# Kernel tuning notes

Measured on AMD Instinct MI355X. Metric: run time of the kernel, lower is better.

The kernel has to match this reference:

```python
import jax, jax.numpy as jnp
import numpy as np

B = 16384        # batch size
K = 50           # neighbors per user (fixed for static shapes)
T = B * K        # total gathered neighbor items
NNEG = 20        # negative samples per positive
D = 128          # embedding dim
N_USERS = 100000
N_ITEMS = 100000
ALPHA = 1.0


def setup_inputs() -> dict:
    key = jax.random.key(0)
    k = jax.random.split(key, 9)
    I = jax.random.randint(k[0], (B,), 0, N_ITEMS)
    U = jax.random.randint(k[1], (B,), 0, N_USERS)
    I_neg = jax.random.randint(k[2], (B, NNEG), 0, N_ITEMS)
    I_U = jax.random.randint(k[3], (T,), 0, N_ITEMS)
    N_U = jnp.full((B,), K, dtype=jnp.int32)
    I_in_I_U = jax.random.randint(k[4], (B,), 0, 2).astype(jnp.int32)
    P_emb = jax.random.normal(k[5], (N_ITEMS, D), jnp.float32) * 0.02
    Q_emb = jax.random.normal(k[6], (N_ITEMS, D), jnp.float32) * 0.02
    b_u = jax.random.normal(k[7], (N_USERS,), jnp.float32) * 0.01
    b_i = jax.random.normal(k[8], (N_ITEMS,), jnp.float32) * 0.01
    return {"I": I, "U": U, "I_neg": I_neg, "I_U": I_U, "N_U": N_U,
            "I_in_I_U": I_in_I_U, "P_emb": P_emb, "Q_emb": Q_emb,
            "b_u": b_u, "b_i": b_i}


def reference(I, U, I_neg, I_U, N_U, I_in_I_U, P_emb, Q_emb, b_u, b_i):
    # P(.) / Q(.) abstracted as embedding lookups
    q = Q_emb[I]                     # [B, D]
    p = P_emb[I_U]                   # [T, D]
    p_self = P_emb[I]                # [B, D]

    # scatter-add neighbor embeddings into per-row sums
    U_idx = jnp.repeat(jnp.arange(B), N_U, total_repeat_length=T)  # [T]
    p_sum = jax.ops.segment_sum(p, U_idx, num_segments=B)          # [B, D]

    ind = I_in_I_U.astype(q.dtype)                                 # [B]
    p_ctx = p_sum - p_self * ind[:, None]                          # exclude self
    div = jnp.clip(N_U.astype(q.dtype) - ind, 1.0, None) ** ALPHA  # [B]
    p_ctx_avg = p_ctx / div[:, None]

    pq = jnp.sum(p_ctx_avg * q, axis=1)                            # [B]
    r = b_u[U] + b_i[I] + pq

    q_neg = Q_emb[I_neg.reshape(-1)].reshape(B, NNEG, D)
    pq_neg = jnp.einsum('bd,bnd->bn', p_ctx_avg, q_neg)            # [B, NNEG]
    r_neg = b_u[U][:, None] + b_i[I_neg] + pq_neg
    return (r, r_neg)
```

## Files before the change

kernel.cpp:

```cpp
#include <hip/hip_runtime.h>


constexpr int B_SZ    = 16384;
constexpr int K_NB    = 50;
constexpr int NNEG    = 20;
constexpr int D_DIM   = 128;
constexpr int N_ITEMS = 100000;

__device__ __forceinline__ uint32_t f2bf_rne(float f) {
    uint32_t u = __float_as_uint(f);
    return (u + 0x7fffu + ((u >> 16) & 1u)) >> 16;
}
__device__ __forceinline__ uint32_t pk2(float lo, float hi) {
    return f2bf_rne(lo) | (f2bf_rne(hi) << 16);
}
__device__ __forceinline__ void unpk2(uint32_t u, float& lo, float& hi) {
    lo = __uint_as_float(u << 16);
    hi = __uint_as_float(u & 0xffff0000u);
}
__device__ __forceinline__ void unpk8(const uint4 v, float* f) {
    unpk2(v.x, f[0], f[1]);
    unpk2(v.y, f[2], f[3]);
    unpk2(v.z, f[4], f[5]);
    unpk2(v.w, f[6], f[7]);
}

__global__ __launch_bounds__(256) void cvt_f32_bf16(
    const float* __restrict__ P, const float* __restrict__ Q,
    uint4* __restrict__ Pb, uint4* __restrict__ Qb, int per_table)
{
    int i = blockIdx.x * blockDim.x + threadIdx.x;
    const float* src; uint4* dst;
    if (i < per_table) { src = P; dst = Pb; }
    else               { src = Q; dst = Qb; i -= per_table; }
    const float4 a = ((const float4*)src)[2 * i];
    const float4 b = ((const float4*)src)[2 * i + 1];
    uint4 o;
    o.x = pk2(a.x, a.y); o.y = pk2(a.z, a.w);
    o.z = pk2(b.x, b.y); o.w = pk2(b.z, b.w);
    dst[i] = o;
}

__global__ __launch_bounds__(256) void fism_fwd_bf16(
    const int* __restrict__ I,
    const int* __restrict__ U,
    const int* __restrict__ I_neg,
    const int* __restrict__ I_U,
    const int* __restrict__ N_U,
    const int* __restrict__ I_in_I_U,
    const ushort* __restrict__ Pb,
    const ushort* __restrict__ Qb,
    const float* __restrict__ b_u,
    const float* __restrict__ b_i,
    float* __restrict__ r,
    float* __restrict__ r_neg)
{
    const int wave = (blockIdx.x * blockDim.x + threadIdx.x) >> 6;
    if (wave >= B_SZ) return;
    const int lane = threadIdx.x & 63;
    const int t    = lane & 15;
    const int g    = lane >> 4;
    const int b    = wave;

    int my_nbr = 0, my_neg = 0;
    if (lane < K_NB) my_nbr = I_U[b * K_NB + lane];
    if (lane < NNEG) my_neg = I_neg[b * NNEG + lane];
    const int   ii  = I[b];
    const int   uu  = U[b];
    const float ind = (float)I_in_I_U[b];
    const float nuf = (float)N_U[b];

    const float bu     = b_u[uu];
    const float bi_pos = b_i[ii];
    float my_bneg = 0.f;
    if (lane < NNEG) my_bneg = b_i[my_neg];

    const uint4 psu = ((const uint4*)(Pb + (size_t)ii * D_DIM))[t];
    const uint4 qpu = ((const uint4*)(Qb + (size_t)ii * D_DIM))[t];

    float acc[8] = {0.f, 0.f, 0.f, 0.f, 0.f, 0.f, 0.f, 0.f};
    #pragma unroll 6
    for (int k = 0; k < K_NB / 4; ++k) {
        const int item = __shfl(my_nbr, 4 * k + g, 64);
        const uint4 v  = ((const uint4*)(Pb + (size_t)item * D_DIM))[t];
        float f[8]; unpk8(v, f);
        #pragma unroll
        for (int j = 0; j < 8; ++j) acc[j] += f[j];
    }
    {
        const int item = __shfl(my_nbr, 48 + (g & 1), 64);
        if (g < 2) {
            const uint4 v = ((const uint4*)(Pb + (size_t)item * D_DIM))[t];
            float f[8]; unpk8(v, f);
            #pragma unroll
            for (int j = 0; j < 8; ++j) acc[j] += f[j];
        }
    }
    #pragma unroll
    for (int j = 0; j < 8; ++j) {
        acc[j] += __shfl_xor(acc[j], 16, 64);
        acc[j] += __shfl_xor(acc[j], 32, 64);
    }

    float ps[8]; unpk8(psu, ps);
    const float inv = 1.0f / fmaxf(nuf - ind, 1.0f);
    float pctx[8];
    #pragma unroll
    for (int j = 0; j < 8; ++j) pctx[j] = (acc[j] - ps[j] * ind) * inv;

    {
        float qp[8]; unpk8(qpu, qp);
        float dot = 0.f;
        #pragma unroll
        for (int j = 0; j < 8; ++j) dot += pctx[j] * qp[j];
        #pragma unroll
        for (int m = 8; m > 0; m >>= 1)
            dot += __shfl_xor(dot, m, 64);
        if (lane == 0) r[b] = bu + bi_pos + dot;
    }

    #pragma unroll
    for (int s = 0; s < NNEG / 4; ++s) {
        const int   n    = 4 * s + g;
        const int   item = __shfl(my_neg,  n, 64);
        const float bn   = __shfl(my_bneg, n, 64);
        const uint4 qv   = ((const uint4*)(Qb + (size_t)item * D_DIM))[t];
        float q8[8]; unpk8(qv, q8);
        float d = 0.f;
        #pragma unroll
        for (int j = 0; j < 8; ++j) d += pctx[j] * q8[j];
        #pragma unroll
        for (int m = 8; m > 0; m >>= 1)
            d += __shfl_xor(d, m, 64);
        if (t == 0) r_neg[b * NNEG + n] = bu + bn + d;
    }
}

__global__ __launch_bounds__(256) void fism_fwd(
    const int* __restrict__ I,
    const int* __restrict__ U,
    const int* __restrict__ I_neg,
    const int* __restrict__ I_U,
    const int* __restrict__ N_U,
    const int* __restrict__ I_in_I_U,
    const float* __restrict__ P,
    const float* __restrict__ Q,
    const float* __restrict__ b_u,
    const float* __restrict__ b_i,
    float* __restrict__ r,
    float* __restrict__ r_neg)
{
    const int wave = (blockIdx.x * blockDim.x + threadIdx.x) >> 6;
    if (wave >= B_SZ) return;
    const int lane = threadIdx.x & 63;
    const int sl   = lane & 31;
    const int half = lane >> 5;
    const int b    = wave;

    int my_nbr = 0, my_neg = 0;
    if (lane < K_NB)  my_nbr = I_U[b * K_NB + lane];
    if (lane < NNEG)  my_neg = I_neg[b * NNEG + lane];
    const int   ii   = I[b];
    const int   uu   = U[b];
    const float ind  = (float)I_in_I_U[b];
    const float nuf  = (float)N_U[b];

    const float bu     = b_u[uu];
    const float bi_pos = b_i[ii];
    float my_bneg = 0.f;
    if (lane < NNEG) my_bneg = b_i[my_neg];

    const float4 ps = ((const float4*)(P + (size_t)ii * D_DIM))[sl];
    const float4 qp = ((const float4*)(Q + (size_t)ii * D_DIM))[sl];

    float4 acc = {0.f, 0.f, 0.f, 0.f};
    #pragma unroll 5
    for (int k = 0; k < K_NB / 2; ++k) {
        const int item = __shfl(my_nbr, 2 * k + half, 64);
        const float4 v = ((const float4*)(P + (size_t)item * D_DIM))[sl];
        acc.x += v.x; acc.y += v.y; acc.z += v.z; acc.w += v.w;
    }
    acc.x += __shfl_xor(acc.x, 32, 64);
    acc.y += __shfl_xor(acc.y, 32, 64);
    acc.z += __shfl_xor(acc.z, 32, 64);
    acc.w += __shfl_xor(acc.w, 32, 64);

    const float inv = 1.0f / fmaxf(nuf - ind, 1.0f);
    float4 pctx;
    pctx.x = (acc.x - ps.x * ind) * inv;
    pctx.y = (acc.y - ps.y * ind) * inv;
    pctx.z = (acc.z - ps.z * ind) * inv;
    pctx.w = (acc.w - ps.w * ind) * inv;

    {
        float dot = pctx.x * qp.x + pctx.y * qp.y + pctx.z * qp.z + pctx.w * qp.w;
        #pragma unroll
        for (int m = 16; m > 0; m >>= 1)
            dot += __shfl_xor(dot, m, 64);
        if (lane == 0) r[b] = bu + bi_pos + dot;
    }

    #pragma unroll 5
    for (int tN = 0; tN < NNEG / 2; ++tN) {
        const int   n    = 2 * tN + half;
        const int   item = __shfl(my_neg,  n, 64);
        const float bn   = __shfl(my_bneg, n, 64);
        const float4 qv  = ((const float4*)(Q + (size_t)item * D_DIM))[sl];
        float d = pctx.x * qv.x + pctx.y * qv.y + pctx.z * qv.z + pctx.w * qv.w;
        #pragma unroll
        for (int m = 16; m > 0; m >>= 1)
            d += __shfl_xor(d, m, 64);
        if (sl == 0) r_neg[b * NNEG + n] = bu + bn + d;
    }
}

extern "C" void kernel_launch(void* const* d_in, const int* in_sizes, int n_in,
                              void* d_out, int out_size, void* d_ws, size_t ws_size,
                              hipStream_t stream) {
    const int*   I        = (const int*)d_in[0];
    const int*   U        = (const int*)d_in[1];
    const int*   I_neg    = (const int*)d_in[2];
    const int*   I_U      = (const int*)d_in[3];
    const int*   N_U      = (const int*)d_in[4];
    const int*   I_in_I_U = (const int*)d_in[5];
    const float* P_emb    = (const float*)d_in[6];
    const float* Q_emb    = (const float*)d_in[7];
    const float* b_u      = (const float*)d_in[8];
    const float* b_i      = (const float*)d_in[9];

    float* r     = (float*)d_out;
    float* r_neg = (float*)d_out + B_SZ;

    const size_t tbl_elems = (size_t)N_ITEMS * D_DIM;
    const size_t need      = 2 * tbl_elems * sizeof(ushort);

    if (d_ws && ws_size >= need) {
        ushort* Pb = (ushort*)d_ws;
        ushort* Qb = Pb + tbl_elems;

        const int per_table   = (int)(tbl_elems / 8);
        const int cvt_blocks  = (2 * per_table) / 256;
        cvt_f32_bf16<<<cvt_blocks, 256, 0, stream>>>(
            P_emb, Q_emb, (uint4*)Pb, (uint4*)Qb, per_table);

        fism_fwd_bf16<<<B_SZ / 4, 256, 0, stream>>>(
            I, U, I_neg, I_U, N_U, I_in_I_U, Pb, Qb, b_u, b_i, r, r_neg);
    } else {
        fism_fwd<<<B_SZ / 4, 256, 0, stream>>>(
            I, U, I_neg, I_U, N_U, I_in_I_U, P_emb, Q_emb, b_u, b_i, r, r_neg);
    }
}
```

Baseline: 187.1 us.

## Batch all gathers up front and narrow per-thread conversion granularity

The main kernel now issues all 13 neighbor-row loads and all 5 negative-item row loads into registers before doing any arithmetic, so more memory requests are in flight per wave. The launch bounds ask for 4 blocks per CU, which limits register use. The conversion kernel now handles one float4 per thread instead of two, doubling the thread count. The risk is higher register pressure, and the occupancy hint could cause spills.

```diff
diff --git a/kernel.cpp b/kernel.cpp
--- a/kernel.cpp
+++ b/kernel.cpp
@@ -26,22 +26,21 @@
 }
 
 __global__ __launch_bounds__(256) void cvt_f32_bf16(
-    const float* __restrict__ P, const float* __restrict__ Q,
-    uint4* __restrict__ Pb, uint4* __restrict__ Qb, int per_table)
+    const float4* __restrict__ P4, const float4* __restrict__ Q4,
+    uint2* __restrict__ Pb2, uint2* __restrict__ Qb2, int per_table4)
 {
     int i = blockIdx.x * blockDim.x + threadIdx.x;
-    const float* src; uint4* dst;
-    if (i < per_table) { src = P; dst = Pb; }
-    else               { src = Q; dst = Qb; i -= per_table; }
-    const float4 a = ((const float4*)src)[2 * i];
-    const float4 b = ((const float4*)src)[2 * i + 1];
-    uint4 o;
-    o.x = pk2(a.x, a.y); o.y = pk2(a.z, a.w);
-    o.z = pk2(b.x, b.y); o.w = pk2(b.z, b.w);
+    const float4* src; uint2* dst;
+    if (i < per_table4) { src = P4; dst = Pb2; }
+    else                { src = Q4; dst = Qb2; i -= per_table4; }
+    const float4 a = src[i];
+    uint2 o;
+    o.x = pk2(a.x, a.y);
+    o.y = pk2(a.z, a.w);
     dst[i] = o;
 }
 
-__global__ __launch_bounds__(256) void fism_fwd_bf16(
+__global__ __launch_bounds__(256, 4) void fism_fwd_bf16(
     const int* __restrict__ I,
     const int* __restrict__ U,
     const int* __restrict__ I_neg,
@@ -78,23 +77,37 @@
     const uint4 psu = ((const uint4*)(Pb + (size_t)ii * D_DIM))[t];
     const uint4 qpu = ((const uint4*)(Qb + (size_t)ii * D_DIM))[t];
 
+    uint4 v[12];
+    #pragma unroll
+    for (int k = 0; k < 12; ++k) {
+        const int item = __shfl(my_nbr, 4 * k + g, 64);
+        v[k] = ((const uint4*)(Pb + (size_t)item * D_DIM))[t];
+    }
+    const int item_t = __shfl(my_nbr, 48 + (g & 1), 64);
+    uint4 vt = {0u, 0u, 0u, 0u};
+    if (g < 2) vt = ((const uint4*)(Pb + (size_t)item_t * D_DIM))[t];
+
+    uint4 qv[5];
+    float bn[5];
+    #pragma unroll
+    for (int s = 0; s < 5; ++s) {
+        const int n = 4 * s + g;
+        const int item = __shfl(my_neg, n, 64);
+        bn[s] = __shfl(my_bneg, n, 64);
+        qv[s] = ((const uint4*)(Qb + (size_t)item * D_DIM))[t];
+    }
+
     float acc[8] = {0.f, 0.f, 0.f, 0.f, 0.f, 0.f, 0.f, 0.f};
-    #pragma unroll 6
-    for (int k = 0; k < K_NB / 4; ++k) {
-        const int item = __shfl(my_nbr, 4 * k + g, 64);
-        const uint4 v  = ((const uint4*)(Pb + (size_t)item * D_DIM))[t];
-        float f[8]; unpk8(v, f);
+    #pragma unroll
+    for (int k = 0; k < 12; ++k) {
+        float f[8]; unpk8(v[k], f);
         #pragma unroll
         for (int j = 0; j < 8; ++j) acc[j] += f[j];
     }
     {
-        const int item = __shfl(my_nbr, 48 + (g & 1), 64);
-        if (g < 2) {
-            const uint4 v = ((const uint4*)(Pb + (size_t)item * D_DIM))[t];
-            float f[8]; unpk8(v, f);
-            #pragma unroll
-            for (int j = 0; j < 8; ++j) acc[j] += f[j];
-        }
+        float f[8]; unpk8(vt, f);
+        #pragma unroll
+        for (int j = 0; j < 8; ++j) acc[j] += f[j];
     }
     #pragma unroll
     for (int j = 0; j < 8; ++j) {
@@ -120,19 +133,15 @@
     }
 
     #pragma unroll
-    for (int s = 0; s < NNEG / 4; ++s) {
-        const int   n    = 4 * s + g;
-        const int   item = __shfl(my_neg,  n, 64);
-        const float bn   = __shfl(my_bneg, n, 64);
-        const uint4 qv   = ((const uint4*)(Qb + (size_t)item * D_DIM))[t];
-        float q8[8]; unpk8(qv, q8);
+    for (int s = 0; s < 5; ++s) {
+        float q8[8]; unpk8(qv[s], q8);
         float d = 0.f;
         #pragma unroll
         for (int j = 0; j < 8; ++j) d += pctx[j] * q8[j];
         #pragma unroll
         for (int m = 8; m > 0; m >>= 1)
             d += __shfl_xor(d, m, 64);
-        if (t == 0) r_neg[b * NNEG + n] = bu + bn + d;
+        if (t == 0) r_neg[b * NNEG + 4 * s + g] = bu + bn[s] + d;
     }
 }
 
@@ -238,10 +247,11 @@
         ushort* Pb = (ushort*)d_ws;
         ushort* Qb = Pb + tbl_elems;
 
-        const int per_table   = (int)(tbl_elems / 8);
-        const int cvt_blocks  = (2 * per_table) / 256;
+        const int per_table4 = (int)(tbl_elems / 4);
+        const int cvt_blocks = (2 * per_table4) / 256;
         cvt_f32_bf16<<<cvt_blocks, 256, 0, stream>>>(
-            P_emb, Q_emb, (uint4*)Pb, (uint4*)Qb, per_table);
+            (const float4*)P_emb, (const float4*)Q_emb,
+            (uint2*)Pb, (uint2*)Qb, per_table4);
 
         fism_fwd_bf16<<<B_SZ / 4, 256, 0, stream>>>(
             I, U, I_neg, I_U, N_U, I_in_I_U, Pb, Qb, b_u, b_i, r, r_neg);
```

Result: no change. 184.8 us (-1.2%).
